# Performance work log

Hardware: AMD Instinct MI355X
Metric: run time of the kernel (lower is better)

The kernel has to match this reference:

```python
import jax, jax.numpy as jnp
import numpy as np

B, S, E, N = 2, 2048, 768, 12
H = E // N

def setup_inputs() -> dict:
    key = jax.random.key(0)
    k1, k2, k3, k4, k5 = jax.random.split(key, 5)
    x = jax.random.normal(k1, (B, S, E), dtype=jnp.float32)
    Wqkv = jax.random.normal(k2, (E, 3 * E), dtype=jnp.float32) * (1.0 / np.sqrt(E))
    bqkv = jax.random.normal(k3, (3 * E,), dtype=jnp.float32) * 0.02
    Wproj = jax.random.normal(k4, (E, E), dtype=jnp.float32) * (1.0 / np.sqrt(E))
    bproj = jax.random.normal(k5, (E,), dtype=jnp.float32) * 0.02
    mask = jnp.tril(jnp.ones((S, S), dtype=jnp.int32))[None, None]  # (1,1,S,S) causal
    return {"mask": mask, "x": x, "Wqkv": Wqkv, "bqkv": bqkv, "Wproj": Wproj, "bproj": bproj}

def reference(mask, x, Wqkv, bqkv, Wproj, bproj):
    Bx, Sx, Ex = x.shape
    Hd = Ex // N
    qkv = x @ Wqkv + bqkv                       # (B,S,3E)
    q, k, v = jnp.split(qkv, 3, axis=-1)
    q = q.reshape(Bx, Sx, N, Hd).transpose(0, 2, 1, 3)  # (B,N,S,H)
    k = k.reshape(Bx, Sx, N, Hd).transpose(0, 2, 1, 3)
    v = v.reshape(Bx, Sx, N, Hd).transpose(0, 2, 1, 3)
    att = jnp.einsum('bnsh,bnth->bnst', q, k) / jnp.sqrt(jnp.float32(Hd))
    att = jnp.where(mask == 0, -jnp.inf, att)   # causal masked_fill
    p = jax.nn.softmax(att, axis=-1)            # dropout p=0.0 -> identity
    y = jnp.einsum('bnst,bnth->bnsh', p, v)     # (B,N,S,H)
    y = y.transpose(0, 2, 1, 3).reshape(Bx, Sx, Ex)
    return y @ Wproj + bproj
```

## Files before the change

kernel.cpp:

```cpp
#include <hip/hip_runtime.h>
#include <hip/hip_bf16.h>
#include <math.h>

#define S_LEN 2048
#define E_DIM 768
#define NHEAD 12
#define HDIM 64
#define BATCH 2
#define MROWS (BATCH * S_LEN)
#define KDIM E_DIM
#define NBN (BATCH * NHEAD)
#define NTASKS 768

#define QSCALE 0.1803368801111204f
#define REF2   11.541560327111707f

typedef __attribute__((ext_vector_type(8))) short bf16x8;
typedef __attribute__((ext_vector_type(4))) float f32x4;

__device__ inline float exp2_fast(float x) {
    return __builtin_amdgcn_exp2f(x);
}

__device__ inline unsigned short f2bf(float f) {
    __hip_bfloat16 h = __float2bfloat16(f);
    union { __hip_bfloat16 b; unsigned short u; } v; v.b = h;
    return v.u;
}

__device__ inline float bf2f(unsigned short u) {
    union { unsigned u32; float f; } v; v.u32 = ((unsigned)u) << 16;
    return v.f;
}

__global__ __launch_bounds__(256) void prep(
    const float* __restrict__ x, unsigned short* __restrict__ Xb,
    const float* __restrict__ Wqkv, unsigned short* __restrict__ WqkvT,
    const float* __restrict__ Wproj, unsigned short* __restrict__ WprojT)
{
    __shared__ float t[32][33];
    const int blk = blockIdx.x, tid = threadIdx.x;
    if (blk < 3072) {
        const int i = blk * 256 + tid;
        const float4 a = ((const float4*)x)[i];
        ushort4 o;
        o.x = f2bf(a.x); o.y = f2bf(a.y); o.z = f2bf(a.z); o.w = f2bf(a.w);
        ((ushort4*)Xb)[i] = o;
        return;
    }
    const float* W; unsigned short* WT; int N, bt;
    if (blk < 3072 + 1728) { bt = blk - 3072; N = 3 * E_DIM; W = Wqkv; WT = WqkvT; }
    else                   { bt = blk - 4800; N = E_DIM;     W = Wproj; WT = WprojT; }
    const int bx = bt % (N / 32), by = bt / (N / 32);
    const int k0 = by * 32, n0 = bx * 32;
    const int r = tid >> 3, c4 = (tid & 7) * 4;
    const float4 v = *(const float4*)&W[(size_t)(k0 + r) * N + n0 + c4];
    t[r][c4 + 0] = v.x; t[r][c4 + 1] = v.y; t[r][c4 + 2] = v.z; t[r][c4 + 3] = v.w;
    __syncthreads();
    ushort4 o;
    o.x = f2bf(t[c4 + 0][r]); o.y = f2bf(t[c4 + 1][r]);
    o.z = f2bf(t[c4 + 2][r]); o.w = f2bf(t[c4 + 3][r]);
    *(ushort4*)&WT[(size_t)(n0 + r) * KDIM + k0 + c4] = o;
}

template <int EPI, int BM, int BN>
__global__ __launch_bounds__(256, 3) void gemm_t(
    const unsigned short* __restrict__ A, const unsigned short* __restrict__ BT,
    const float* __restrict__ bias, void* __restrict__ out0,
    void* __restrict__ out1, void* __restrict__ out2, int Nn)
{
    constexpr int MF = BM / 32;
    constexpr int NF = BN / 32;
    __shared__ unsigned short As[BM * 64];
    __shared__ unsigned short Bs[BN * 64];
    const int tid = threadIdx.x;
    const int lane = tid & 63;
    const int wid = tid >> 6;
    const int lr = lane & 15, lg = lane >> 4;
    const int wr = wid >> 1, wc = wid & 1;
    const int m0 = blockIdx.y * BM;
    const int n0 = blockIdx.x * BN;
    const int srow = lane >> 3, scol = (lane & 7) * 8;

    f32x4 acc[MF][NF];
    #pragma unroll
    for (int i = 0; i < MF; ++i)
        #pragma unroll
        for (int j = 0; j < NF; ++j) acc[i][j] = (f32x4){0.f, 0.f, 0.f, 0.f};

    for (int k0 = 0; k0 < KDIM; k0 += 64) {
        __syncthreads();
        #pragma unroll
        for (int c = 0; c < MF; ++c) {
            const int chunk = wid * MF + c;
            const int row = chunk * 8 + srow;
            const unsigned short* ga = A + (size_t)(m0 + row) * KDIM + k0 + scol;
            __builtin_amdgcn_global_load_lds(
                (const __attribute__((address_space(1))) void*)ga,
                (__attribute__((address_space(3))) void*)&As[chunk * 512], 16, 0, 0);
        }
        #pragma unroll
        for (int c = 0; c < NF; ++c) {
            const int chunk = wid * NF + c;
            const int row = chunk * 8 + srow;
            const unsigned short* gb = BT + (size_t)(n0 + row) * KDIM + k0 + scol;
            __builtin_amdgcn_global_load_lds(
                (const __attribute__((address_space(1))) void*)gb,
                (__attribute__((address_space(3))) void*)&Bs[chunk * 512], 16, 0, 0);
        }
        __syncthreads();

        #pragma unroll
        for (int kk = 0; kk < 2; ++kk) {
            bf16x8 af[MF], bf[NF];
            #pragma unroll
            for (int mt = 0; mt < MF; ++mt)
                af[mt] = *(const bf16x8*)&As[(wr * (BM / 2) + mt * 16 + lr) * 64 + kk * 32 + lg * 8];
            #pragma unroll
            for (int nt = 0; nt < NF; ++nt)
                bf[nt] = *(const bf16x8*)&Bs[(wc * (BN / 2) + nt * 16 + lr) * 64 + kk * 32 + lg * 8];
            #pragma unroll
            for (int mt = 0; mt < MF; ++mt)
                #pragma unroll
                for (int nt = 0; nt < NF; ++nt)
                    acc[mt][nt] = __builtin_amdgcn_mfma_f32_16x16x32_bf16(
                        af[mt], bf[nt], acc[mt][nt], 0, 0, 0);
        }
    }

    #pragma unroll
    for (int mt = 0; mt < MF; ++mt) {
        const int rowbase = m0 + wr * (BM / 2) + mt * 16 + lg * 4;
        #pragma unroll
        for (int nt = 0; nt < NF; ++nt) {
            const int col = n0 + wc * (BN / 2) + nt * 16 + lr;
            if (EPI == 0) {
                float* O = (float*)out0;
                const float bv = bias[col];
                #pragma unroll
                for (int r = 0; r < 4; ++r)
                    O[(size_t)(rowbase + r) * Nn + col] = acc[mt][nt][r] + bv;
            } else {
                const int which = col / E_DIM;
                const int rem = col % E_DIM;
                const int head = rem >> 6, h = rem & 63;
                const float bv = bias[col];
                if (which == 2) {
                    const int b = rowbase >> 11, s0 = rowbase & (S_LEN - 1);
                    const int scolv = (s0 & ~63) | ((s0 & 63) ^ ((h & 7) << 3));
                    unsigned short* VT = (unsigned short*)out2;
                    ushort4 pk;
                    pk.x = f2bf(acc[mt][nt][0] + bv);
                    pk.y = f2bf(acc[mt][nt][1] + bv);
                    pk.z = f2bf(acc[mt][nt][2] + bv);
                    pk.w = f2bf(acc[mt][nt][3] + bv);
                    *(ushort4*)&VT[((size_t)(b * NHEAD + head) * HDIM + h) * S_LEN + scolv] = pk;
                } else {
                    unsigned short* dst = (which == 0) ? (unsigned short*)out0
                                                       : (unsigned short*)out1;
                    const float sc = (which == 0) ? QSCALE : 1.0f;
                    #pragma unroll
                    for (int r = 0; r < 4; ++r) {
                        const int m = rowbase + r;
                        const int b = m >> 11, s = m & (S_LEN - 1);
                        const int hh = (which == 1) ? (h ^ ((s & 7) << 3)) : h;
                        dst[(((size_t)(b * NHEAD + head) * S_LEN) + s) * HDIM + hh] =
                            f2bf((acc[mt][nt][r] + bv) * sc);
                    }
                }
            }
        }
    }
}

__global__ __launch_bounds__(256, 4) void attn_mfma(
    const unsigned short* __restrict__ Qb, const unsigned short* __restrict__ Kb,
    const unsigned short* __restrict__ VTb, unsigned short* __restrict__ Y,
    unsigned short* __restrict__ ws_o, float* __restrict__ ws_l)
{
    __shared__ unsigned short smem[5 * 4096];

    const int tid = threadIdx.x;
    const int lane = tid & 63;
    const int wid = tid >> 6;
    const int lr = lane & 15;
    const int lg = lane >> 4;

    unsigned short* const Pw = smem + 16384 + wid * 1024;

    const short one_bf = (short)0x3F80;
    bf16x8 onesB;
    #pragma unroll
    for (int j = 0; j < 8; ++j) onesB[j] = one_bf;

    const int B = blockIdx.x;
    const int xcd = B & 7, slot = B >> 3;
    const int bn = xcd + (slot >> 5) * 8;
    const int rest = slot & 31;
    const int jj = rest & 15, half = rest >> 4;
    const int b = bn / NHEAD, n = bn % NHEAD;

    const unsigned short* Kg = Kb + (size_t)bn * S_LEN * HDIM;
    const unsigned short* Vg = VTb + (size_t)bn * HDIM * S_LEN;

    auto run_pass = [&](int qb, int t0, int t1, int mode) {
        const size_t qoff = ((size_t)bn * S_LEN + (qb * 64 + wid * 16 + lr)) * HDIM;
        const bf16x8 qB0 = *(const bf16x8*)(Qb + qoff + lg * 8);
        const bf16x8 qB1 = *(const bf16x8*)(Qb + qoff + 32 + lg * 8);

        f32x4 o[4];
        #pragma unroll
        for (int ht = 0; ht < 4; ++ht) o[ht] = (f32x4){0.f, 0.f, 0.f, 0.f};
        f32x4 lsum = (f32x4){0.f, 0.f, 0.f, 0.f};

        __syncthreads();
        #pragma unroll
        for (int e = 0; e < 2; ++e) {
            const int chunk = wid * 2 + e;
            __builtin_amdgcn_global_load_lds(
                (const __attribute__((address_space(1))) void*)
                    (Kg + (size_t)t0 * 4096 + chunk * 512 + lane * 8),
                (__attribute__((address_space(3))) void*)&smem[chunk * 512], 16, 0, 0);
            __builtin_amdgcn_global_load_lds(
                (const __attribute__((address_space(1))) void*)
                    (Vg + (size_t)(chunk * 8 + (lane >> 3)) * S_LEN + t0 * 64 + (lane & 7) * 8),
                (__attribute__((address_space(3))) void*)&smem[8192 + chunk * 512], 16, 0, 0);
        }

        int cur = 0;
        for (int t = t0; t < t1; ++t) {
            __syncthreads();
            if (t + 1 < t1) {
                #pragma unroll
                for (int e = 0; e < 2; ++e) {
                    const int chunk = wid * 2 + e;
                    __builtin_amdgcn_global_load_lds(
                        (const __attribute__((address_space(1))) void*)
                            (Kg + (size_t)(t + 1) * 4096 + chunk * 512 + lane * 8),
                        (__attribute__((address_space(3))) void*)
                            &smem[(cur ^ 1) * 4096 + chunk * 512], 16, 0, 0);
                    __builtin_amdgcn_global_load_lds(
                        (const __attribute__((address_space(1))) void*)
                            (Vg + (size_t)(chunk * 8 + (lane >> 3)) * S_LEN + (t + 1) * 64
                                + (lane & 7) * 8),
                        (__attribute__((address_space(3))) void*)
                            &smem[8192 + (cur ^ 1) * 4096 + chunk * 512], 16, 0, 0);
                }
            }

            const unsigned short* Kc = smem + cur * 4096;
            const unsigned short* Vc = smem + 8192 + cur * 4096;

            f32x4 s[4];
            __builtin_amdgcn_s_setprio(1);
            #pragma unroll
            for (int ct = 0; ct < 4; ++ct) {
                const int kr = ct * 16 + lr;
                const int xo = (kr & 7) << 3;
                const bf16x8 kb0 = *(const bf16x8*)&Kc[kr * 64 + ((lg * 8) ^ xo)];
                const bf16x8 kb1 = *(const bf16x8*)&Kc[kr * 64 + ((32 + lg * 8) ^ xo)];
                f32x4 a = (f32x4){0.f, 0.f, 0.f, 0.f};
                a = __builtin_amdgcn_mfma_f32_16x16x32_bf16(kb0, qB0, a, 0, 0, 0);
                a = __builtin_amdgcn_mfma_f32_16x16x32_bf16(kb1, qB1, a, 0, 0, 0);
                s[ct] = a;
            }
            __builtin_amdgcn_s_setprio(0);

            if (t == qb) {
                const int q = qb * 64 + wid * 16 + lr;
                #pragma unroll
                for (int ct = 0; ct < 4; ++ct) {
                    #pragma unroll
                    for (int r = 0; r < 4; ++r) {
                        const int k = t * 64 + ct * 16 + lg * 4 + r;
                        if (k > q) s[ct][r] = -1e30f;
                    }
                }
            }

            const int pxo = (lr & 7) << 3;
            #pragma unroll
            for (int ct = 0; ct < 4; ++ct) {
                const float p0 = exp2_fast(s[ct][0] - REF2);
                const float p1 = exp2_fast(s[ct][1] - REF2);
                const float p2 = exp2_fast(s[ct][2] - REF2);
                const float p3 = exp2_fast(s[ct][3] - REF2);
                ushort4 pk;
                pk.x = f2bf(p0); pk.y = f2bf(p1); pk.z = f2bf(p2); pk.w = f2bf(p3);
                *(ushort4*)&Pw[lr * 64 + ((ct * 16 + lg * 4) ^ pxo)] = pk;
            }

            const bf16x8 pa0 = *(const bf16x8*)&Pw[lr * 64 + ((lg * 8) ^ pxo)];
            const bf16x8 pa1 = *(const bf16x8*)&Pw[lr * 64 + ((32 + lg * 8) ^ pxo)];
            __builtin_amdgcn_s_setprio(1);
            lsum = __builtin_amdgcn_mfma_f32_16x16x32_bf16(pa0, onesB, lsum, 0, 0, 0);
            lsum = __builtin_amdgcn_mfma_f32_16x16x32_bf16(pa1, onesB, lsum, 0, 0, 0);
            #pragma unroll
            for (int ht = 0; ht < 4; ++ht) {
                const int h = ht * 16 + lr;
                const int xo = (h & 7) << 3;
                const bf16x8 vb0 = *(const bf16x8*)&Vc[h * 64 + ((lg * 8) ^ xo)];
                const bf16x8 vb1 = *(const bf16x8*)&Vc[h * 64 + ((32 + lg * 8) ^ xo)];
                o[ht] = __builtin_amdgcn_mfma_f32_16x16x32_bf16(pa0, vb0, o[ht], 0, 0, 0);
                o[ht] = __builtin_amdgcn_mfma_f32_16x16x32_bf16(pa1, vb1, o[ht], 0, 0, 0);
            }
            __builtin_amdgcn_s_setprio(0);
            cur ^= 1;
        }

        if (mode == 2) {
            float invl[4];
            #pragma unroll
            for (int r = 0; r < 4; ++r) invl[r] = 1.f / lsum[r];
            #pragma unroll
            for (int r = 0; r < 4; ++r) {
                const int qrow = qb * 64 + wid * 16 + lg * 4 + r;
                unsigned short* yrow =
                    Y + ((size_t)(b * S_LEN + qrow)) * E_DIM + n * HDIM;
                #pragma unroll
                for (int ht = 0; ht < 4; ++ht)
                    yrow[ht * 16 + lr] = f2bf(o[ht][r] * invl[r]);
            }
        } else {
            const size_t m = (size_t)(bn * 16 + (qb - 16)) * 2 + mode;
            unsigned short* wo = ws_o + m * 4096;
            const int rowl = wid * 16 + lg * 4;
            #pragma unroll
            for (int ht = 0; ht < 4; ++ht)
                #pragma unroll
                for (int r = 0; r < 4; ++r)
                    wo[(rowl + r) * 64 + ht * 16 + lr] = f2bf(o[ht][r]);
            if (lr == 0) {
                #pragma unroll
                for (int r = 0; r < 4; ++r)
                    ws_l[m * 64 + rowl + r] = lsum[r];
            }
        }
    };

    if (half == 0) {
        run_pass(31 - jj, 0, 16, 0);
    } else {
        run_pass(31 - jj, 16, 32 - jj, 1);
        run_pass(jj, 0, jj + 1, 2);
    }
}

__global__ __launch_bounds__(256) void attn_merge(
    const unsigned short* __restrict__ ws_o, const float* __restrict__ ws_l,
    unsigned short* __restrict__ Y)
{
    const int m = blockIdx.x;
    const int bn = m / 16, qb = 16 + (m % 16);
    const int b = bn / NHEAD, n = bn % NHEAD;
    const int tid = threadIdx.x;
    const int r = tid >> 2, h0 = (tid & 3) * 16;

    const unsigned short* o0 = ws_o + ((size_t)m * 2 + 0) * 4096 + r * 64 + h0;
    const unsigned short* o1 = ws_o + ((size_t)m * 2 + 1) * 4096 + r * 64 + h0;
    const float l = ws_l[((size_t)m * 2 + 0) * 64 + r] +
                    ws_l[((size_t)m * 2 + 1) * 64 + r];
    const float inv = 1.f / l;
    unsigned short* yrow =
        Y + ((size_t)(b * S_LEN + qb * 64 + r)) * E_DIM + n * HDIM + h0;
    #pragma unroll
    for (int q = 0; q < 16; q += 4) {
        const ushort4 a = *(const ushort4*)(o0 + q);
        const ushort4 c = *(const ushort4*)(o1 + q);
        ushort4 pk;
        pk.x = f2bf((bf2f(a.x) + bf2f(c.x)) * inv);
        pk.y = f2bf((bf2f(a.y) + bf2f(c.y)) * inv);
        pk.z = f2bf((bf2f(a.z) + bf2f(c.z)) * inv);
        pk.w = f2bf((bf2f(a.w) + bf2f(c.w)) * inv);
        *(ushort4*)&yrow[q] = pk;
    }
}

extern "C" void kernel_launch(void* const* d_in, const int* in_sizes, int n_in,
                              void* d_out, int out_size, void* d_ws, size_t ws_size,
                              hipStream_t stream) {
    const float* x     = (const float*)d_in[1];
    const float* Wqkv  = (const float*)d_in[2];
    const float* bqkv  = (const float*)d_in[3];
    const float* Wproj = (const float*)d_in[4];
    const float* bproj = (const float*)d_in[5];
    float* out = (float*)d_out;

    const size_t per = (size_t)BATCH * NHEAD * S_LEN * HDIM;
    unsigned short* Xb     = (unsigned short*)d_ws;
    unsigned short* WqkvT  = Xb + (size_t)MROWS * E_DIM;
    unsigned short* WprojT = WqkvT + (size_t)3 * E_DIM * E_DIM;
    unsigned short* Qb     = WprojT + (size_t)E_DIM * E_DIM;
    unsigned short* Kb     = Qb + per;
    unsigned short* VTb    = Kb + per;
    unsigned short* Yb     = VTb + per;
    unsigned short* ws_o   = Yb + (size_t)MROWS * E_DIM;
    float*          ws_l   = (float*)(ws_o + (size_t)384 * 2 * 4096);

    prep<<<5376, 256, 0, stream>>>(x, Xb, Wqkv, WqkvT, Wproj, WprojT);
    gemm_t<1, 128, 96><<<dim3(3 * E_DIM / 96, MROWS / 128), 256, 0, stream>>>(
        Xb, WqkvT, bqkv, Qb, Kb, VTb, 3 * E_DIM);
    attn_mfma<<<NTASKS, 256, 0, stream>>>(Qb, Kb, VTb, Yb, ws_o, ws_l);
    attn_merge<<<384, 256, 0, stream>>>(ws_o, ws_l, Yb);
    gemm_t<0, 64, 64><<<dim3(E_DIM / 64, MROWS / 64), 256, 0, stream>>>(
        Yb, WprojT, bproj, out, nullptr, nullptr, E_DIM);
}
```

Baseline: 77.69 us.

## Halve attention KV tile to 32 keys to double occupancy

Shrinks the K/V tile processed per iteration from 64 to 32 keys. This halves LDS use per block (smem buffers and the P scratch) and raises launch_bounds min blocks from 4 to 8 so more waves can hide latency. The V-transpose swizzle in the QKV GEMM epilogue and the LDS swizzles are adapted to the 32-wide rows, and the causal loop bounds and mask condition are rescaled. The cost is twice as many loop iterations and barriers, with less MFMA work between each sync.

```diff
diff --git a/kernel.cpp b/kernel.cpp
--- a/kernel.cpp
+++ b/kernel.cpp
@@ -147,7 +147,7 @@
                 const float bv = bias[col];
                 if (which == 2) {
                     const int b = rowbase >> 11, s0 = rowbase & (S_LEN - 1);
-                    const int scolv = (s0 & ~63) | ((s0 & 63) ^ ((h & 7) << 3));
+                    const int scolv = (s0 & ~31) | ((s0 & 31) ^ (((h >> 1) & 3) << 3));
                     unsigned short* VT = (unsigned short*)out2;
                     ushort4 pk;
                     pk.x = f2bf(acc[mt][nt][0] + bv);
@@ -173,12 +173,12 @@
     }
 }
 
-__global__ __launch_bounds__(256, 4) void attn_mfma(
+__global__ __launch_bounds__(256, 8) void attn_mfma(
     const unsigned short* __restrict__ Qb, const unsigned short* __restrict__ Kb,
     const unsigned short* __restrict__ VTb, unsigned short* __restrict__ Y,
     unsigned short* __restrict__ ws_o, float* __restrict__ ws_l)
 {
-    __shared__ unsigned short smem[5 * 4096];
+    __shared__ unsigned short smem[10240];
 
     const int tid = threadIdx.x;
     const int lane = tid & 63;
@@ -186,7 +186,7 @@
     const int lr = lane & 15;
     const int lg = lane >> 4;
 
-    unsigned short* const Pw = smem + 16384 + wid * 1024;
+    unsigned short* const Pw = smem + 8192 + wid * 512;
 
     const short one_bf = (short)0x3F80;
     bf16x8 onesB;
@@ -203,6 +203,9 @@
     const unsigned short* Kg = Kb + (size_t)bn * S_LEN * HDIM;
     const unsigned short* Vg = VTb + (size_t)bn * HDIM * S_LEN;
 
+    const int ksr = lane >> 3, ksc = (lane & 7) * 8;
+    const int vsr = lane >> 2, vsc = (lane & 3) * 8;
+
     auto run_pass = [&](int qb, int t0, int t1, int mode) {
         const size_t qoff = ((size_t)bn * S_LEN + (qb * 64 + wid * 16 + lr)) * HDIM;
         const bf16x8 qB0 = *(const bf16x8*)(Qb + qoff + lg * 8);
@@ -214,47 +217,40 @@
         f32x4 lsum = (f32x4){0.f, 0.f, 0.f, 0.f};
 
         __syncthreads();
-        #pragma unroll
-        for (int e = 0; e < 2; ++e) {
-            const int chunk = wid * 2 + e;
+        {
             __builtin_amdgcn_global_load_lds(
                 (const __attribute__((address_space(1))) void*)
-                    (Kg + (size_t)t0 * 4096 + chunk * 512 + lane * 8),
-                (__attribute__((address_space(3))) void*)&smem[chunk * 512], 16, 0, 0);
+                    (Kg + (size_t)t0 * 2048 + wid * 512 + lane * 8),
+                (__attribute__((address_space(3))) void*)&smem[wid * 512], 16, 0, 0);
             __builtin_amdgcn_global_load_lds(
                 (const __attribute__((address_space(1))) void*)
-                    (Vg + (size_t)(chunk * 8 + (lane >> 3)) * S_LEN + t0 * 64 + (lane & 7) * 8),
-                (__attribute__((address_space(3))) void*)&smem[8192 + chunk * 512], 16, 0, 0);
+                    (Vg + (size_t)(wid * 16 + vsr) * S_LEN + t0 * 32 + vsc),
+                (__attribute__((address_space(3))) void*)&smem[4096 + wid * 512], 16, 0, 0);
         }
 
         int cur = 0;
         for (int t = t0; t < t1; ++t) {
             __syncthreads();
             if (t + 1 < t1) {
-                #pragma unroll
-                for (int e = 0; e < 2; ++e) {
-                    const int chunk = wid * 2 + e;
-                    __builtin_amdgcn_global_load_lds(
-                        (const __attribute__((address_space(1))) void*)
-                            (Kg + (size_t)(t + 1) * 4096 + chunk * 512 + lane * 8),
-                        (__attribute__((address_space(3))) void*)
-                            &smem[(cur ^ 1) * 4096 + chunk * 512], 16, 0, 0);
-                    __builtin_amdgcn_global_load_lds(
-                        (const __attribute__((address_space(1))) void*)
-                            (Vg + (size_t)(chunk * 8 + (lane >> 3)) * S_LEN + (t + 1) * 64
-                                + (lane & 7) * 8),
-                        (__attribute__((address_space(3))) void*)
-                            &smem[8192 + (cur ^ 1) * 4096 + chunk * 512], 16, 0, 0);
-                }
-            }
-
-            const unsigned short* Kc = smem + cur * 4096;
-            const unsigned short* Vc = smem + 8192 + cur * 4096;
-
-            f32x4 s[4];
+                __builtin_amdgcn_global_load_lds(
+                    (const __attribute__((address_space(1))) void*)
+                        (Kg + (size_t)(t + 1) * 2048 + wid * 512 + lane * 8),
+                    (__attribute__((address_space(3))) void*)
+                        &smem[(cur ^ 1) * 2048 + wid * 512], 16, 0, 0);
+                __builtin_amdgcn_global_load_lds(
+                    (const __attribute__((address_space(1))) void*)
+                        (Vg + (size_t)(wid * 16 + vsr) * S_LEN + (t + 1) * 32 + vsc),
+                    (__attribute__((address_space(3))) void*)
+                        &smem[4096 + (cur ^ 1) * 2048 + wid * 512], 16, 0, 0);
+            }
+
+            const unsigned short* Kc = smem + cur * 2048;
+            const unsigned short* Vc = smem + 4096 + cur * 2048;
+
+            f32x4 s[2];
             __builtin_amdgcn_s_setprio(1);
             #pragma unroll
-            for (int ct = 0; ct < 4; ++ct) {
+            for (int ct = 0; ct < 2; ++ct) {
                 const int kr = ct * 16 + lr;
                 const int xo = (kr & 7) << 3;
                 const bf16x8 kb0 = *(const bf16x8*)&Kc[kr * 64 + ((lg * 8) ^ xo)];
@@ -266,43 +262,39 @@
             }
             __builtin_amdgcn_s_setprio(0);
 
-            if (t == qb) {
+            if (t >= 2 * qb) {
                 const int q = qb * 64 + wid * 16 + lr;
                 #pragma unroll
-                for (int ct = 0; ct < 4; ++ct) {
+                for (int ct = 0; ct < 2; ++ct) {
                     #pragma unroll
                     for (int r = 0; r < 4; ++r) {
-                        const int k = t * 64 + ct * 16 + lg * 4 + r;
+                        const int k = t * 32 + ct * 16 + lg * 4 + r;
                         if (k > q) s[ct][r] = -1e30f;
                     }
                 }
             }
 
-            const int pxo = (lr & 7) << 3;
-            #pragma unroll
-            for (int ct = 0; ct < 4; ++ct) {
+            const int pxo = ((lr >> 1) & 3) << 3;
+            #pragma unroll
+            for (int ct = 0; ct < 2; ++ct) {
                 const float p0 = exp2_fast(s[ct][0] - REF2);
                 const float p1 = exp2_fast(s[ct][1] - REF2);
                 const float p2 = exp2_fast(s[ct][2] - REF2);
                 const float p3 = exp2_fast(s[ct][3] - REF2);
                 ushort4 pk;
                 pk.x = f2bf(p0); pk.y = f2bf(p1); pk.z = f2bf(p2); pk.w = f2bf(p3);
-                *(ushort4*)&Pw[lr * 64 + ((ct * 16 + lg * 4) ^ pxo)] = pk;
-            }
-
-            const bf16x8 pa0 = *(const bf16x8*)&Pw[lr * 64 + ((lg * 8) ^ pxo)];
-            const bf16x8 pa1 = *(const bf16x8*)&Pw[lr * 64 + ((32 + lg * 8) ^ pxo)];
+                *(ushort4*)&Pw[lr * 32 + ((ct * 16 + lg * 4) ^ pxo)] = pk;
+            }
+
+            const bf16x8 pa = *(const bf16x8*)&Pw[lr * 32 + ((lg * 8) ^ pxo)];
             __builtin_amdgcn_s_setprio(1);
-            lsum = __builtin_amdgcn_mfma_f32_16x16x32_bf16(pa0, onesB, lsum, 0, 0, 0);
-            lsum = __builtin_amdgcn_mfma_f32_16x16x32_bf16(pa1, onesB, lsum, 0, 0, 0);
+            lsum = __builtin_amdgcn_mfma_f32_16x16x32_bf16(pa, onesB, lsum, 0, 0, 0);
             #pragma unroll
             for (int ht = 0; ht < 4; ++ht) {
                 const int h = ht * 16 + lr;
-                const int xo = (h & 7) << 3;
-                const bf16x8 vb0 = *(const bf16x8*)&Vc[h * 64 + ((lg * 8) ^ xo)];
-                const bf16x8 vb1 = *(const bf16x8*)&Vc[h * 64 + ((32 + lg * 8) ^ xo)];
-                o[ht] = __builtin_amdgcn_mfma_f32_16x16x32_bf16(pa0, vb0, o[ht], 0, 0, 0);
-                o[ht] = __builtin_amdgcn_mfma_f32_16x16x32_bf16(pa1, vb1, o[ht], 0, 0, 0);
+                const int vxo = (((h >> 1) & 3) << 3);
+                const bf16x8 vb = *(const bf16x8*)&Vc[h * 32 + ((lg * 8) ^ vxo)];
+                o[ht] = __builtin_amdgcn_mfma_f32_16x16x32_bf16(pa, vb, o[ht], 0, 0, 0);
             }
             __builtin_amdgcn_s_setprio(0);
             cur ^= 1;
@@ -339,10 +331,10 @@
     };
 
     if (half == 0) {
-        run_pass(31 - jj, 0, 16, 0);
+        run_pass(31 - jj, 0, 32, 0);
     } else {
-        run_pass(31 - jj, 16, 32 - jj, 1);
-        run_pass(jj, 0, jj + 1, 2);
+        run_pass(31 - jj, 32, 64 - 2 * jj, 1);
+        run_pass(jj, 0, 2 * jj + 2, 2);
     }
 }
 
```

New measurement: 81.91 us. +5.4%, slower.
